# Kernel optimization log

Hardware: AMD Instinct MI355X
Metric: run time of the kernel (lower is better)

Reference implementation:

```python
import jax, jax.numpy as jnp
import numpy as np

N_HEADS = 8
N_LAYERS = 2
LN_EPS = 1e-5


def _mha(x, Win, bin_, Wout, bout):
    # torch nn.MultiheadAttention, eval mode (dropout off). x: [b, s, d]
    b, s, d = x.shape
    dh = d // N_HEADS
    qkv = x @ Win.T + bin_                      # [b, s, 3d]
    q, k, v = jnp.split(qkv, 3, axis=-1)
    q = q.reshape(b, s, N_HEADS, dh)
    k = k.reshape(b, s, N_HEADS, dh)
    v = v.reshape(b, s, N_HEADS, dh)
    scores = jnp.einsum('bqhd,bkhd->bhqk', q, k) / jnp.sqrt(jnp.asarray(dh, x.dtype))
    attn = jax.nn.softmax(scores, axis=-1)
    o = jnp.einsum('bhqk,bkhd->bqhd', attn, v).reshape(b, s, d)
    return o @ Wout.T + bout


def _layer_norm(x, g, b):
    mu = jnp.mean(x, axis=-1, keepdims=True)
    var = jnp.mean(jnp.square(x - mu), axis=-1, keepdims=True)
    return (x - mu) * jax.lax.rsqrt(var + LN_EPS) * g + b


def _vertex_conv(feat, inc, prev, Win, bin_, Wout, bout, Wproj, ln_g, ln_b, alpha):
    # feat: [b,m,d], inc: [b,m,e]
    attn = _mha(feat, Win, bin_, Wout, bout)              # [b,m,d]
    scores = jnp.einsum('bme,bmd->bed', inc, attn)        # incidence aggregation
    w = jax.nn.softmax(scores, axis=1)                    # softmax over edges
    # fused form of einsum('bme,bmd->bmed') then einsum('bmed,bed->bed')
    edge = scores * w                                     # [b,e,d]
    edge = edge @ Wproj.T                                 # no-bias projection
    edge = _layer_norm(edge, ln_g, ln_b)
    if prev is not None:
        edge = alpha * prev + (1.0 - alpha) * edge
        edge = edge + prev
    return edge


def _edge_conv(inc, edge_feat, prev, Win, bin_, Wout, bout, Wproj, ln_g, ln_b, alpha):
    # inc: [b,m,e], edge_feat: [b,e,d]
    _ = _mha(edge_feat, Win, bin_, Wout, bout)            # attn computed, output unused downstream
    wef = jnp.einsum('bed,bme->bmd', edge_feat, inc)      # edge->node aggregation
    node = wef @ Wproj.T
    node = _layer_norm(node, ln_g, ln_b)
    if prev is not None:
        node = alpha * prev + (1.0 - alpha) * node
        node = node + prev
    return node


def setup_inputs() -> dict:
    key = jax.random.key(0)
    ks = jax.random.split(key, 8)
    b, m, e, d = 8, 1024, 1536, 256
    s = 0.02
    return {
        'features': jax.random.normal(ks[0], (b, m, d), jnp.float32),
        'inc_mat': (jax.random.uniform(ks[1], (b, m, e), jnp.float32) < 0.05).astype(jnp.float32),
        'vc_Win': jax.random.normal(ks[2], (3 * d, d), jnp.float32) * s,
        'vc_bin': jnp.zeros((3 * d,), jnp.float32),
        'vc_Wout': jax.random.normal(ks[3], (d, d), jnp.float32) * s,
        'vc_bout': jnp.zeros((d,), jnp.float32),
        'vc_Wproj': jax.random.normal(ks[4], (d, d), jnp.float32) * s,
        'vc_ln_g': jnp.ones((d,), jnp.float32),
        'vc_ln_b': jnp.zeros((d,), jnp.float32),
        'vc_alpha': jnp.asarray(0.5, jnp.float32),
        'ec_Win': jax.random.normal(ks[5], (3 * d, d), jnp.float32) * s,
        'ec_bin': jnp.zeros((3 * d,), jnp.float32),
        'ec_Wout': jax.random.normal(ks[6], (d, d), jnp.float32) * s,
        'ec_bout': jnp.zeros((d,), jnp.float32),
        'ec_Wproj': jax.random.normal(ks[7], (d, d), jnp.float32) * s,
        'ec_ln_g': jnp.ones((d,), jnp.float32),
        'ec_ln_b': jnp.zeros((d,), jnp.float32),
        'ec_alpha': jnp.asarray(0.5, jnp.float32),
    }


def reference(features, inc_mat,
              vc_Win, vc_bin, vc_Wout, vc_bout, vc_Wproj, vc_ln_g, vc_ln_b, vc_alpha,
              ec_Win, ec_bin, ec_Wout, ec_bout, ec_Wproj, ec_ln_g, ec_ln_b, ec_alpha):
    vc = (vc_Win, vc_bin, vc_Wout, vc_bout, vc_Wproj, vc_ln_g, vc_ln_b, vc_alpha)
    ec = (ec_Win, ec_bin, ec_Wout, ec_bout, ec_Wproj, ec_ln_g, ec_ln_b, ec_alpha)
    edge_feats = _vertex_conv(features, inc_mat, None, *vc)
    node_feats = _edge_conv(inc_mat, edge_feats, features, *ec)
    for _ in range(N_LAYERS):  # shared weights across layers, as in the torch module
        edge_feats = _vertex_conv(features, inc_mat, edge_feats, *vc)
        node_feats = _edge_conv(inc_mat, edge_feats, node_feats, *ec)
    return node_feats, edge_feats, inc_mat
```

## Files before the change

### kernel.cpp

```cpp
#include <hip/hip_runtime.h>
#include <stdint.h>


#define DEV static __device__ __forceinline__

typedef __attribute__((ext_vector_type(8))) short bf16x8;
typedef __attribute__((ext_vector_type(4))) float f32x4;

DEV uint16_t f2bf(float x){
  union{float f; uint32_t u;} v; v.f=x;
  uint32_t r = v.u + 0x7fffu + ((v.u>>16)&1u);
  return (uint16_t)(r>>16);
}
DEV float bf2f(uint16_t b){
  union{uint32_t u; float f;} v; v.u=((uint32_t)b)<<16; return v.f;
}

DEV uint32_t cvtpk_bf16(float lo, float hi){
  uint32_t d;
  asm("v_cvt_pk_bf16_f32 %0, %1, %2" : "=v"(d) : "v"(lo), "v"(hi));
  return d;
}

#if __has_builtin(__builtin_amdgcn_exp2f)
DEV float exp2fast(float x){ return __builtin_amdgcn_exp2f(x); }
#else
DEV float exp2fast(float x){ return __expf(x * 0.6931471805599453f); }
#endif

#if __has_builtin(__builtin_amdgcn_global_load_lds)
#define HAVE_GLL 1
#else
#define HAVE_GLL 0
#endif

DEV void load_lds16(const uint16_t* g, void* l){
#if HAVE_GLL
  __builtin_amdgcn_global_load_lds((const __attribute__((address_space(1))) uint32_t*)g,
                                   (__attribute__((address_space(3))) uint32_t*)l, 16, 0, 0);
#else
  *(bf16x8*)l = *(const bf16x8*)g;
#endif
}

__global__ __launch_bounds__(256, 3)
void qkv_prep(const float* __restrict__ inc, float* __restrict__ out_inc,
              uint16_t* __restrict__ incb, uint16_t* __restrict__ incT,
              const float* __restrict__ feats, const float* __restrict__ win,
              const float* __restrict__ bias, uint16_t* __restrict__ qkvb,
              const float* __restrict__ wout, const float* __restrict__ wpv,
              const float* __restrict__ wpe,
              uint16_t* __restrict__ ob_w, uint16_t* __restrict__ ov_w,
              uint16_t* __restrict__ oe_w){
  __shared__ union {
    struct { short As[128*32]; short Bs[128*32]; } g;
    float T[64*65];
  } sm;
  const int tid = threadIdx.x;
  const int bx = blockIdx.x;

  if (bx < 384){
    const int lane = tid & 63;
    const int w = tid >> 6;
    const int wm = w & 1, wn = w >> 1;
    const int r = lane & 15, q = lane >> 4;
    const int mtile = bx & 63, ntile = bx >> 6;
    const float* Fb = feats + (size_t)(mtile*128)*256;
    const float* Wb = win + (size_t)(ntile*128)*256;
    f32x4 acc[4][4];
#pragma unroll
    for (int i=0;i<4;++i)
#pragma unroll
      for (int j=0;j<4;++j) acc[i][j] = (f32x4){0.f,0.f,0.f,0.f};

    const int srow = tid >> 2;
    const int sblk = tid & 3;

    for (int kb = 0; kb < 256; kb += 32){
#pragma unroll
      for (int i=0;i<2;++i){
        int row = srow + 64*i;
        const float* src = Fb + (size_t)row*256 + kb + sblk*8;
        float4 a0 = *(const float4*)src;
        float4 a1 = *(const float4*)(src+4);
        union{uint32_t u[4]; bf16x8 v8;} pk;
        pk.u[0]=cvtpk_bf16(a0.x,a0.y); pk.u[1]=cvtpk_bf16(a0.z,a0.w);
        pk.u[2]=cvtpk_bf16(a1.x,a1.y); pk.u[3]=cvtpk_bf16(a1.z,a1.w);
        *(bf16x8*)&sm.g.As[row*32 + (sblk ^ (row&3))*8] = pk.v8;
      }
#pragma unroll
      for (int i=0;i<2;++i){
        int row = srow + 64*i;
        const float* src = Wb + (size_t)row*256 + kb + sblk*8;
        float4 a0 = *(const float4*)src;
        float4 a1 = *(const float4*)(src+4);
        union{uint32_t u[4]; bf16x8 v8;} pk;
        pk.u[0]=cvtpk_bf16(a0.x,a0.y); pk.u[1]=cvtpk_bf16(a0.z,a0.w);
        pk.u[2]=cvtpk_bf16(a1.x,a1.y); pk.u[3]=cvtpk_bf16(a1.z,a1.w);
        *(bf16x8*)&sm.g.Bs[row*32 + (sblk ^ (row&3))*8] = pk.v8;
      }
      __syncthreads();
      bf16x8 af[4], bfr[4];
#pragma unroll
      for (int mt=0;mt<4;++mt){
        int m = wm*64 + mt*16 + r;
        af[mt] = *(const bf16x8*)&sm.g.As[m*32 + (q ^ (m&3))*8];
      }
#pragma unroll
      for (int nt=0;nt<4;++nt){
        int n = wn*64 + nt*16 + r;
        bfr[nt] = *(const bf16x8*)&sm.g.Bs[n*32 + (q ^ (n&3))*8];
      }
#pragma unroll
      for (int mt=0;mt<4;++mt)
#pragma unroll
        for (int nt=0;nt<4;++nt)
          acc[mt][nt] = __builtin_amdgcn_mfma_f32_16x16x32_bf16(af[mt], bfr[nt], acc[mt][nt], 0,0,0);
      __syncthreads();
    }

    const int gm0 = mtile*128 + wm*64;
    const int gn0 = ntile*128 + wn*64;
#pragma unroll
    for (int mt=0;mt<4;++mt){
#pragma unroll
      for (int nt=0;nt<4;++nt){
        int gn = gn0 + nt*16 + r;
        float bv = bias[gn];
#pragma unroll
        for (int reg=0;reg<4;++reg){
          int gm = gm0 + mt*16 + q*4 + reg;
          qkvb[(size_t)gm*768 + gn] = f2bf(acc[mt][nt][reg] + bv);
        }
      }
    }
  } else if (bx < 3456){
    int p = bx - 384;
    int x = p % 24;
    int t = p / 24;
    int y = t & 15;
    int b = t >> 4;
    int c0 = x*64, r0 = y*64;
    int tx = tid & 15, ty = tid >> 4;
    size_t base = (size_t)b*1024*1536;
#pragma unroll
    for (int jj=0;jj<4;++jj){
      int rl = ty + jj*16;
      size_t idx = base + (size_t)(r0+rl)*1536 + c0 + tx*4;
      float4 v = *(const float4*)&inc[idx];
      *(float4*)&out_inc[idx] = v;
      union{uint16_t u[4]; uint64_t q64;} pk;
      pk.u[0]=f2bf(v.x); pk.u[1]=f2bf(v.y); pk.u[2]=f2bf(v.z); pk.u[3]=f2bf(v.w);
      *(uint64_t*)&incb[idx] = pk.q64;
      float* Tp = &sm.T[rl*65 + tx*4];
      Tp[0]=v.x; Tp[1]=v.y; Tp[2]=v.z; Tp[3]=v.w;
    }
    __syncthreads();
    int c = tid >> 2, ms = (tid & 3) * 16;
    size_t baseT = (size_t)b*1536*1024;
    uint16_t* dst = incT + baseT + (size_t)(c0+c)*1024 + r0 + ms;
    union{uint16_t u[8]; uint4 v4;} o0, o1;
#pragma unroll
    for (int j=0;j<8;++j) o0.u[j] = f2bf(sm.T[(ms+j)*65 + c]);
#pragma unroll
    for (int j=0;j<8;++j) o1.u[j] = f2bf(sm.T[(ms+8+j)*65 + c]);
    *(uint4*)dst = o0.v4;
    *(uint4*)(dst+8) = o1.v4;
  } else {
    int i = (bx - 3456)*256 + tid;
    const float* src; uint16_t* dst; int j;
    if (i < 16384){ src=wout; dst=ob_w; j=i; }
    else if (i < 32768){ src=wpv; dst=ov_w; j=i-16384; }
    else { src=wpe; dst=oe_w; j=i-32768; }
    float4 v = ((const float4*)src)[j];
    union { uint16_t u[4]; uint64_t q; } p;
    p.u[0]=f2bf(v.x); p.u[1]=f2bf(v.y); p.u[2]=f2bf(v.z); p.u[3]=f2bf(v.w);
    ((uint64_t*)dst)[j] = p.q;
  }
}

template<int WM, int BK, int EPI>
__global__ __launch_bounds__(256, 3)
void gemm_nt(const uint16_t* __restrict__ A, const uint16_t* __restrict__ B,
             uint16_t* __restrict__ Cb, const float* __restrict__ bias,
             int M, int N, int K){
  constexpr int AROWS = WM*32;
  constexpr int UPR = BK/8;
  constexpr int RPP = 256/UPR;
  __shared__ short As[AROWS*BK];
  __shared__ short Bs[128*BK];
  const int tid = threadIdx.x;
  const int lane = tid & 63;
  const int w = tid >> 6;
  const int wm = w & 1, wn = w >> 1;
  const int r = lane & 15, q = lane >> 4;
  const uint16_t* Ab = A + (size_t)(blockIdx.x*AROWS)*K;
  const uint16_t* Bb = B + (size_t)(blockIdx.y*128)*K;
  f32x4 acc[WM][4];
#pragma unroll
  for (int i=0;i<WM;++i)
#pragma unroll
    for (int j=0;j<4;++j) acc[i][j] = (f32x4){0.f,0.f,0.f,0.f};

  const int srow = tid / UPR;
  const int sblk = tid % UPR;

  for (int kb = 0; kb < K; kb += BK){
#pragma unroll
    for (int i=0;i<AROWS/RPP;++i){
      int row = srow + RPP*i;
      int lblk = sblk ^ (row & (UPR-1));
      load_lds16(Ab + (size_t)row*K + kb + lblk*8, (char*)As + i*4096 + tid*16);
    }
#pragma unroll
    for (int i=0;i<128/RPP;++i){
      int row = srow + RPP*i;
      int lblk = sblk ^ (row & (UPR-1));
      load_lds16(Bb + (size_t)row*K + kb + lblk*8, (char*)Bs + i*4096 + tid*16);
    }
    __syncthreads();
#pragma unroll
    for (int kc=0;kc<BK/32;++kc){
      bf16x8 af[WM], bfr[4];
#pragma unroll
      for (int mt=0;mt<WM;++mt){
        int m = wm*(WM*16) + mt*16 + r;
        af[mt] = *(const bf16x8*)&As[m*BK + ((kc*4 + q) ^ (m&(UPR-1)))*8];
      }
#pragma unroll
      for (int nt=0;nt<4;++nt){
        int n = wn*64 + nt*16 + r;
        bfr[nt] = *(const bf16x8*)&Bs[n*BK + ((kc*4 + q) ^ (n&(UPR-1)))*8];
      }
#pragma unroll
      for (int mt=0;mt<WM;++mt)
#pragma unroll
        for (int nt=0;nt<4;++nt)
          acc[mt][nt] = __builtin_amdgcn_mfma_f32_16x16x32_bf16(af[mt], bfr[nt], acc[mt][nt], 0,0,0);
    }
    __syncthreads();
  }

  const int gm0 = blockIdx.x*AROWS + wm*(WM*16);
  const int gn0 = blockIdx.y*128 + wn*64;

  if constexpr (EPI == 1){
#pragma unroll
    for (int mt=0;mt<WM;++mt){
      int gmb = gm0 + mt*16 + q*4;
      size_t bb_ = (size_t)(gmb>>10)*(256*1024);
      int mm = gmb & 1023;
#pragma unroll
      for (int nt=0;nt<4;++nt){
        int gn = gn0 + nt*16 + r;
        float bv = bias ? bias[gn] : 0.f;
        union{uint16_t u[4]; uint64_t q64;} pk;
#pragma unroll
        for (int reg=0;reg<4;++reg) pk.u[reg] = f2bf(acc[mt][nt][reg] + bv);
        *(uint64_t*)(Cb + bb_ + (size_t)gn*1024 + mm) = pk.q64;
      }
    }
  } else {
#pragma unroll
    for (int mt=0;mt<WM;++mt){
#pragma unroll
      for (int nt=0;nt<4;++nt){
        int gn = gn0 + nt*16 + r;
        float bv = bias ? bias[gn] : 0.f;
#pragma unroll
        for (int reg=0;reg<4;++reg){
          int gm = gm0 + mt*16 + q*4 + reg;
          Cb[(size_t)gm*N + gn] = f2bf(acc[mt][nt][reg] + bv);
        }
      }
    }
  }
}

__global__ __launch_bounds__(256, 4)
void gemm_score(const uint16_t* __restrict__ A,
                const uint16_t* __restrict__ B,
                float* __restrict__ part,
                uint16_t* __restrict__ VE){
  __shared__ short As[32*64];
  __shared__ short Bs[128*64];
  const int tid = threadIdx.x;
  const int lane = tid & 63;
  const int w = tid >> 6;
  const int r = lane & 15, q = lane >> 4;
  const int bx = (blockIdx.x & 7)*96 + (blockIdx.x >> 3);
  const int batch = bx / 96;
  const int t = bx % 96;
  const int etile = t >> 1, dh = t & 1;
  const uint16_t* Ab = A + (size_t)(batch*1536 + etile*32)*1024;
  const uint16_t* Bb = B + (size_t)(batch*256 + dh*128)*1024;

  f32x4 acc[2][2];
#pragma unroll
  for (int i=0;i<2;++i)
#pragma unroll
    for (int j=0;j<2;++j) acc[i][j] = (f32x4){0.f,0.f,0.f,0.f};

  const int srow = tid >> 3;
  const int sblk = tid & 7;

  for (int kb = 0; kb < 1024; kb += 64){
    { int lblk = sblk ^ (srow & 7);
      load_lds16(Ab + (size_t)srow*1024 + kb + lblk*8, (char*)As + tid*16); }
#pragma unroll
    for (int i=0;i<4;++i){
      int row = srow + 32*i;
      int lblk = sblk ^ (row & 7);
      load_lds16(Bb + (size_t)row*1024 + kb + lblk*8, (char*)Bs + i*4096 + tid*16);
    }
    __syncthreads();
#pragma unroll
    for (int kc=0;kc<2;++kc){
      bf16x8 af[2], bfr[2];
#pragma unroll
      for (int mt=0;mt<2;++mt){
        int m = mt*16 + r;
        af[mt] = *(const bf16x8*)&As[m*64 + ((kc*4 + q) ^ (m&7))*8];
      }
#pragma unroll
      for (int nt=0;nt<2;++nt){
        int n = w*32 + nt*16 + r;
        bfr[nt] = *(const bf16x8*)&Bs[n*64 + ((kc*4 + q) ^ (n&7))*8];
      }
#pragma unroll
      for (int mt=0;mt<2;++mt)
#pragma unroll
        for (int nt=0;nt<2;++nt)
          acc[mt][nt] = __builtin_amdgcn_mfma_f32_16x16x32_bf16(af[mt], bfr[nt], acc[mt][nt], 0,0,0);
    }
    __syncthreads();
  }

  const size_t er0 = (size_t)batch*1536 + etile*32;
#pragma unroll
  for (int nt=0;nt<2;++nt){
    int gn = dh*128 + w*32 + nt*16 + r;
    float s = 0.f;
#pragma unroll
    for (int mt=0;mt<2;++mt){
#pragma unroll
      for (int reg=0;reg<4;++reg){
        float v = acc[mt][nt][reg];
        float ev = __expf(v);
        s += ev;
        int row = mt*16 + q*4 + reg;
        VE[(er0 + row)*256 + gn] = f2bf(v*ev);
      }
    }
    s += __shfl_xor(s, 16);
    s += __shfl_xor(s, 32);
    if (q == 0) part[(size_t)(batch*48 + etile)*256 + gn] = s;
  }
}

__global__ __launch_bounds__(256, 4)
void gemm_ln_edge(const uint16_t* __restrict__ SB, const uint16_t* __restrict__ B,
                  const float* __restrict__ part, const float* __restrict__ g,
                  const float* __restrict__ bb, const float* __restrict__ alpha,
                  float* __restrict__ out, uint16_t* __restrict__ baset){
  __shared__ short As[16*64];
  __shared__ short Bs[256*64];
  __shared__ float lnS[4][16], lnQ[4][16];
  __shared__ float PLinv[256];
  const int tid = threadIdx.x;
  const int lane = tid & 63;
  const int w = tid >> 6;
  const int r = lane & 15, q = lane >> 4;
  const int bx = (blockIdx.x & 7)*96 + (blockIdx.x >> 3);
  const int batch = bx / 96;

  {
    float s = 0.f;
#pragma unroll
    for (int i=0;i<48;++i) s += part[((size_t)batch*48 + i)*256 + tid];
    PLinv[tid] = 1.0f / s;
  }
  __syncthreads();

  f32x4 acc[4];
#pragma unroll
  for (int j=0;j<4;++j) acc[j] = (f32x4){0.f,0.f,0.f,0.f};

  const int srow = tid >> 3;
  const int sblk = tid & 7;

  for (int kb = 0; kb < 256; kb += 64){
    if (tid < 128){
      bf16x8 v = *(const bf16x8*)(SB + (size_t)(bx*16 + srow)*256 + kb + sblk*8);
      const float* Lp = &PLinv[kb + sblk*8];
      float xv[8];
#pragma unroll
      for (int j=0;j<8;++j) xv[j] = bf2f((uint16_t)v[j]) * Lp[j];
      union{uint32_t u[4]; bf16x8 v8;} pk;
      pk.u[0] = cvtpk_bf16(xv[0], xv[1]);
      pk.u[1] = cvtpk_bf16(xv[2], xv[3]);
      pk.u[2] = cvtpk_bf16(xv[4], xv[5]);
      pk.u[3] = cvtpk_bf16(xv[6], xv[7]);
      *(bf16x8*)&As[srow*64 + (sblk ^ (srow&7))*8] = pk.v8;
    }
#pragma unroll
    for (int i=0;i<8;++i){
      int row = srow + 32*i;
      int lblk = sblk ^ (row & 7);
      load_lds16(B + (size_t)row*256 + kb + lblk*8, (char*)Bs + i*4096 + tid*16);
    }
    __syncthreads();
#pragma unroll
    for (int kc=0;kc<2;++kc){
      bf16x8 af, bfr[4];
      { int m = r;
        af = *(const bf16x8*)&As[m*64 + ((kc*4 + q) ^ (m&7))*8]; }
#pragma unroll
      for (int nt=0;nt<4;++nt){
        int n = w*64 + nt*16 + r;
        bfr[nt] = *(const bf16x8*)&Bs[n*64 + ((kc*4 + q) ^ (n&7))*8];
      }
#pragma unroll
      for (int nt=0;nt<4;++nt)
        acc[nt] = __builtin_amdgcn_mfma_f32_16x16x32_bf16(af, bfr[nt], acc[nt], 0,0,0);
    }
    __syncthreads();
  }

  float rs[4], rq[4];
#pragma unroll
  for (int reg=0;reg<4;++reg){
    float s=0.f, s2=0.f;
#pragma unroll
    for (int nt=0;nt<4;++nt){
      float v = acc[nt][reg];
      s += v; s2 += v*v;
    }
#pragma unroll
    for (int off=1; off<16; off<<=1){ s += __shfl_xor(s,off); s2 += __shfl_xor(s2,off); }
    rs[reg]=s; rq[reg]=s2;
  }
  if (r == 0){
#pragma unroll
    for (int reg=0;reg<4;++reg){
      int row = q*4 + reg;
      lnS[w][row] = rs[reg];
      lnQ[w][row] = rq[reg];
    }
  }
  __syncthreads();

  const float c0 = 3.0f + alpha[0];
  float mu_[4], rstd_[4];
#pragma unroll
  for (int reg=0;reg<4;++reg){
    int row = q*4 + reg;
    float S = lnS[0][row]+lnS[1][row]+lnS[2][row]+lnS[3][row];
    float Q = lnQ[0][row]+lnQ[1][row]+lnQ[2][row]+lnQ[3][row];
    float mu = S * (1.f/256.f);
    float var = fmaxf(Q*(1.f/256.f) - mu*mu, 0.f);
    mu_[reg] = mu;
    rstd_[reg] = rsqrtf(var + 1e-5f);
  }

  int e0 = (bx % 96) * 16;
#pragma unroll
  for (int nt=0;nt<4;++nt){
    int gn = w*64 + nt*16 + r;
    float gv = g[gn], bv = bb[gn];
    union{uint16_t u[4]; uint64_t q64;} pk;
#pragma unroll
    for (int reg=0;reg<4;++reg){
      int row = q*4 + reg;
      size_t gm = (size_t)bx*16 + row;
      float o = ((acc[nt][reg]-mu_[reg])*rstd_[reg]*gv + bv) * c0;
      pk.u[reg] = f2bf(o);
      out[gm*256 + gn] = o;
    }
    int ee = e0 + q*4;
    *(uint64_t*)(baset + ((size_t)batch*256 + gn)*1536 + ee) = pk.q64;
  }
}

__global__ __launch_bounds__(256, 3)
void gemm_node_fused(const uint16_t* __restrict__ inc,
                     const uint16_t* __restrict__ baset,
                     const uint16_t* __restrict__ wpe,
                     const float* __restrict__ g, const float* __restrict__ bb,
                     const float* __restrict__ alpha,
                     const float* __restrict__ feats, float* __restrict__ out){
  __shared__ short Ws[256*64];
  __shared__ short As2[16*256];
  __shared__ short Is[16*64];
  const int tid = threadIdx.x;
  const int lane = tid & 63;
  const int w = tid >> 6;
  const int r = lane & 15, q = lane >> 4;
  const int bx = (blockIdx.x & 7)*64 + (blockIdx.x >> 3);
  const int batch = bx >> 6;
  const int mt0 = (bx & 63) * 16;

  const int srow = tid >> 3;
  const int sblk = tid & 7;

  const uint16_t* Bb = baset + (size_t)batch*256*1536;
  const uint16_t* Ib = inc + ((size_t)batch*1024 + mt0)*1536;

  f32x4 acc1[4];
#pragma unroll
  for (int i=0;i<4;++i) acc1[i] = (f32x4){0.f,0.f,0.f,0.f};

  for (int kb = 0; kb < 1536; kb += 64){
#pragma unroll
    for (int i=0;i<8;++i){
      int row = srow + 32*i;
      int lblk = sblk ^ (row & 7);
      load_lds16(Bb + (size_t)row*1536 + kb + lblk*8, (char*)Ws + i*4096 + tid*16);
    }
    if (tid < 128){
      int lblk = sblk ^ (srow & 7);
      load_lds16(Ib + (size_t)srow*1536 + kb + lblk*8, (char*)Is + tid*16);
    }
    __syncthreads();
#pragma unroll
    for (int kc=0;kc<2;++kc){
      bf16x8 af[4], bfr;
#pragma unroll
      for (int mt=0;mt<4;++mt){
        int d = w*64 + mt*16 + r;
        af[mt] = *(const bf16x8*)&Ws[d*64 + ((kc*4 + q) ^ (d&7))*8];
      }
      { int m = r;
        bfr = *(const bf16x8*)&Is[m*64 + ((kc*4 + q) ^ (m&7))*8]; }
#pragma unroll
      for (int mt=0;mt<4;++mt)
        acc1[mt] = __builtin_amdgcn_mfma_f32_16x16x32_bf16(af[mt], bfr, acc1[mt], 0,0,0);
    }
    __syncthreads();
  }

#pragma unroll
  for (int mt=0;mt<4;++mt){
    int j = w*8 + mt*2 + (q>>1);
    int m = r;
    union{uint16_t u[4]; uint64_t q64;} pk;
#pragma unroll
    for (int reg=0;reg<4;++reg) pk.u[reg] = f2bf(acc1[mt][reg]);
    *(uint64_t*)((char*)As2 + m*512 + ((j ^ (m&7))<<4) + ((q&1)<<3)) = pk.q64;
  }

  f32x4 acc2[4];
#pragma unroll
  for (int i=0;i<4;++i) acc2[i] = (f32x4){0.f,0.f,0.f,0.f};

  for (int kb = 0; kb < 256; kb += 64){
#pragma unroll
    for (int i=0;i<8;++i){
      int row = srow + 32*i;
      int lblk = sblk ^ (row & 7);
      load_lds16(wpe + (size_t)row*256 + kb + lblk*8, (char*)Ws + i*4096 + tid*16);
    }
    __syncthreads();
#pragma unroll
    for (int kc=0;kc<2;++kc){
      bf16x8 af[4], bfr;
#pragma unroll
      for (int mt=0;mt<4;++mt){
        int dp = w*64 + mt*16 + r;
        af[mt] = *(const bf16x8*)&Ws[dp*64 + ((kc*4 + q) ^ (dp&7))*8];
      }
      { int m = r;
        int jr = (kb>>3) + kc*4 + q;
        bfr = *(const bf16x8*)((char*)As2 + m*512 + ((jr ^ (m&7))<<4)); }
#pragma unroll
      for (int mt=0;mt<4;++mt)
        acc2[mt] = __builtin_amdgcn_mfma_f32_16x16x32_bf16(af[mt], bfr, acc2[mt], 0,0,0);
    }
    __syncthreads();
  }

  float* lnS = (float*)Is;
  float* lnQ = lnS + 64;
  float s_, q_;
  {
    float s=0.f, s2=0.f;
#pragma unroll
    for (int mt=0;mt<4;++mt)
#pragma unroll
      for (int reg=0;reg<4;++reg){
        float v = acc2[mt][reg];
        s += v; s2 += v*v;
      }
    s += __shfl_xor(s,16); s2 += __shfl_xor(s2,16);
    s += __shfl_xor(s,32); s2 += __shfl_xor(s2,32);
    s_ = s; q_ = s2;
  }
  if (q == 0){
    lnS[w*16 + r] = s_;
    lnQ[w*16 + r] = q_;
  }
  __syncthreads();

  const float a = alpha[0];
  const float ap1 = 1.f + a;
  const float cn = (1.f - a)*(ap1*ap1 + ap1 + 1.f);
  const float cf = ap1*ap1*ap1;

  float mu_, rstd_;
  {
    int col = r;
    float S = lnS[col] + lnS[16+col] + lnS[32+col] + lnS[48+col];
    float Q = lnQ[col] + lnQ[16+col] + lnQ[32+col] + lnQ[48+col];
    float mu = S * (1.f/256.f);
    float var = fmaxf(Q*(1.f/256.f) - mu*mu, 0.f);
    mu_ = mu;
    rstd_ = rsqrtf(var + 1e-5f);
  }

#pragma unroll
  for (int mt=0;mt<4;++mt){
    int dp0 = w*64 + mt*16 + q*4;
    float4 gv = *(const float4*)&g[dp0];
    float4 bv = *(const float4*)&bb[dp0];
    int m = r;
    size_t gm = (size_t)batch*1024 + mt0 + m;
    float4 fv = *(const float4*)&feats[gm*256 + dp0];
    float4 ov;
    ov.x = cf*fv.x + cn*((acc2[mt][0]-mu_)*rstd_*gv.x + bv.x);
    ov.y = cf*fv.y + cn*((acc2[mt][1]-mu_)*rstd_*gv.y + bv.y);
    ov.z = cf*fv.z + cn*((acc2[mt][2]-mu_)*rstd_*gv.z + bv.z);
    ov.w = cf*fv.w + cn*((acc2[mt][3]-mu_)*rstd_*gv.w + bv.w);
    *(float4*)&out[gm*256 + dp0] = ov;
  }
}

DEV void stage_K(short* Kl, const uint16_t* __restrict__ qkv, size_t rowbase,
                 int c, int h, int kr){
  const uint16_t* kp = qkv + ((rowbase + c*256 + kr)*768 + 256 + h*32);
  int sz = (kr&3) ^ ((kr>>2)&1);
#pragma unroll
  for (int lb=0; lb<4; ++lb){
    bf16x8 v = *(const bf16x8*)(kp + lb*8);
    *(bf16x8*)&Kl[kr*32 + ((lb ^ sz))*8] = v;
  }
}

DEV void stage_V(short* VT, const uint16_t* __restrict__ qkv, size_t rowbase,
                 int c, int h, int t){
  int kvp = (t>>1)*2;
  int dhh = (t&1)*16;
  const uint16_t* v0 = qkv + ((rowbase + c*256 + kvp)*768 + 512 + h*32 + dhh);
  const uint16_t* v1 = v0 + 768;
  bf16x8 a0 = *(const bf16x8*)(v0);
  bf16x8 a1 = *(const bf16x8*)(v0+8);
  bf16x8 b0 = *(const bf16x8*)(v1);
  bf16x8 b1 = *(const bf16x8*)(v1+8);
  int blkbase = kvp>>3, off = kvp&7;
#pragma unroll
  for (int i=0;i<8;++i){
    int dh = dhh + i;
    uint32_t pack = (uint32_t)(uint16_t)a0[i] | ((uint32_t)(uint16_t)b0[i]<<16);
    *(uint32_t*)&VT[dh*256 + ((blkbase ^ (dh&7))*8) + off] = pack;
  }
#pragma unroll
  for (int i=0;i<8;++i){
    int dh = dhh + 8 + i;
    uint32_t pack = (uint32_t)(uint16_t)a1[i] | ((uint32_t)(uint16_t)b1[i]<<16);
    *(uint32_t*)&VT[dh*256 + ((blkbase ^ (dh&7))*8) + off] = pack;
  }
}

__global__ __launch_bounds__(512)
void attn_fwd(const uint16_t* __restrict__ qkv, uint16_t* __restrict__ O){
  __shared__ short Kl[256*32];
  __shared__ short VT[32*256];
  __shared__ short Pl[8][16*36];
  const int tid = threadIdx.x, lane = tid&63, w = tid>>6;
  const int r = lane&15, q = lane>>4;
  const int logical = (blockIdx.x & 7)*64 + (blockIdx.x >> 3);
  const int bh = logical >> 3, qc = logical & 7;
  const int b = bh>>3, h = bh&7;
  const int q0 = qc*128 + w*16;
  const size_t rowbase = (size_t)b*1024;

  bf16x8 aq;
  {
    const float qscale = 0.25505654380651023f;
    const uint16_t* p = qkv + ((rowbase + q0 + r)*768 + h*32 + q*8);
    bf16x8 t = *(const bf16x8*)p;
#pragma unroll
    for (int j=0;j<8;++j)
      t[j] = (short)f2bf(bf2f((uint16_t)t[j]) * qscale);
    aq = t;
  }

  f32x4 o[2];
  o[0]=(f32x4){0.f,0.f,0.f,0.f}; o[1]=(f32x4){0.f,0.f,0.f,0.f};
  float l = 0.f;

  for (int c=0;c<4;++c){
    __syncthreads();
    if (tid < 256) stage_K(Kl, qkv, rowbase, c, h, tid);
    else           stage_V(VT, qkv, rowbase, c, h, tid-256);
    __syncthreads();
    for (int s32=0; s32<8; ++s32){
#pragma unroll
      for (int t2=0;t2<2;++t2){
        int rn = s32*32 + t2*16 + r;
        int sz = (rn&3) ^ ((rn>>2)&1);
        bf16x8 bk = *(const bf16x8*)&Kl[rn*32 + ((q ^ sz))*8];
        f32x4 z = (f32x4){0.f,0.f,0.f,0.f};
        __builtin_amdgcn_s_setprio(1);
        f32x4 st = __builtin_amdgcn_mfma_f32_16x16x32_bf16(bk, aq, z, 0,0,0);
        __builtin_amdgcn_s_setprio(0);
        float p0 = exp2fast(st[0]);
        float p1 = exp2fast(st[1]);
        float p2 = exp2fast(st[2]);
        float p3 = exp2fast(st[3]);
        l += (p0+p1)+(p2+p3);
        union{uint32_t u[2]; uint64_t q64;} pk;
        pk.u[0] = cvtpk_bf16(p0, p1);
        pk.u[1] = cvtpk_bf16(p2, p3);
        *(uint64_t*)&Pl[w][r*36 + t2*16 + q*4] = pk.q64;
      }
      bf16x8 bv[2];
#pragma unroll
      for (int db=0;db<2;++db){
        int dh = db*16 + r;
        bv[db] = *(const bf16x8*)&VT[dh*256 + (((s32*4 + q) ^ (dh&7)))*8];
      }
      bf16x8 ap = *(const bf16x8*)&Pl[w][r*36 + q*8];
      __builtin_amdgcn_s_setprio(1);
#pragma unroll
      for (int db=0;db<2;++db)
        o[db] = __builtin_amdgcn_mfma_f32_16x16x32_bf16(ap, bv[db], o[db], 0,0,0);
      __builtin_amdgcn_s_setprio(0);
    }
  }

  l += __shfl_xor(l, 16);
  l += __shfl_xor(l, 32);
#pragma unroll
  for (int db=0;db<2;++db)
#pragma unroll
    for (int reg=0;reg<4;++reg){
      float li = __shfl(l, q*4 + reg);
      int qr = q0 + q*4 + reg;
      O[(rowbase + qr)*256 + h*32 + db*16 + r] = f2bf(o[db][reg] / li);
    }
}

extern "C" void kernel_launch(void* const* d_in, const int* in_sizes, int n_in,
                              void* d_out, int out_size, void* d_ws, size_t ws_size,
                              hipStream_t stream){
  const float* features = (const float*)d_in[0];
  const float* inc      = (const float*)d_in[1];
  const float* vc_Win   = (const float*)d_in[2];
  const float* vc_bin   = (const float*)d_in[3];
  const float* vc_Wout  = (const float*)d_in[4];
  const float* vc_bout  = (const float*)d_in[5];
  const float* vc_Wproj = (const float*)d_in[6];
  const float* vc_ln_g  = (const float*)d_in[7];
  const float* vc_ln_b  = (const float*)d_in[8];
  const float* vc_alpha = (const float*)d_in[9];
  const float* ec_Wproj = (const float*)d_in[14];
  const float* ec_ln_g  = (const float*)d_in[15];
  const float* ec_ln_b  = (const float*)d_in[16];
  const float* ec_alpha = (const float*)d_in[17];

  float* out = (float*)d_out;
  float* out_node = out;
  float* out_edge = out + 2097152;
  float* out_inc  = out + 5242880;

  char* ws = (char*)d_ws;
  float*    PART   = (float*)   (ws + 0);
  uint16_t* WOUTB  = (uint16_t*)(ws + 4587520);
  uint16_t* WPVB   = (uint16_t*)(ws + 4718592);
  uint16_t* WPEB   = (uint16_t*)(ws + 4849664);
  uint16_t* INCB   = (uint16_t*)(ws + 4988928);
  uint16_t* INCT   = (uint16_t*)(ws + 30154752);
  uint16_t* QKVB   = (uint16_t*)(ws + 55320576);
  uint16_t* SCORESB= (uint16_t*)(ws + 55320576);
  uint16_t* OB     = (uint16_t*)(ws + 67903488);
  uint16_t* ATTNT  = (uint16_t*)(ws + 72097792);
  uint16_t* BASET  = (uint16_t*)(ws + 82583552);

  qkv_prep<<<3648,256,0,stream>>>(inc, out_inc, INCB, INCT,
                                  features, vc_Win, vc_bin, QKVB,
                                  vc_Wout, vc_Wproj, ec_Wproj,
                                  WOUTB, WPVB, WPEB);

  attn_fwd<<<512,512,0,stream>>>(QKVB, OB);
  gemm_nt<2,128,1><<<dim3(128,2,1),256,0,stream>>>(OB, WOUTB, ATTNT, vc_bout,
                                                   8192,256,256);

  gemm_score<<<768,256,0,stream>>>(INCT, ATTNT, PART, SCORESB);

  gemm_ln_edge<<<768,256,0,stream>>>(SCORESB, WPVB, PART, vc_ln_g, vc_ln_b,
                                     vc_alpha, out_edge, BASET);

  gemm_node_fused<<<512,256,0,stream>>>(INCB, BASET, WPEB, ec_ln_g, ec_ln_b,
                                        ec_alpha, features, out_node);
}
```

Measured before the change: 242.1 us.

## Reassociate out-projection after incidence aggregation and fuse into score GEMM

Drops the separate out-projection GEMM. The incidence aggregation now multiplies the attention output O directly, (inc^T O) Wout^T, and the bias term is recovered as column sums of inc times bout. Those column sums are computed in the prep kernel, and attn_fwd writes O transposed through LDS. The score kernel chains two MFMA GEMMs per 16-edge tile, so the per-block B tile doubles to 256 columns. This removes one launch and the ATTNT round trip, in exchange for extra K=256 GEMM work per edge tile and a larger LDS footprint.

New measurement: 251.4 us. 3.8% more time.

```diff
diff --git a/kernel.cpp b/kernel.cpp
--- a/kernel.cpp
+++ b/kernel.cpp
@@ -51,7 +51,8 @@
               const float* __restrict__ wout, const float* __restrict__ wpv,
               const float* __restrict__ wpe,
               uint16_t* __restrict__ ob_w, uint16_t* __restrict__ ov_w,
-              uint16_t* __restrict__ oe_w){
+              uint16_t* __restrict__ oe_w,
+              float* __restrict__ incpart){
   __shared__ union {
     struct { short As[128*32]; short Bs[128*32]; } g;
     float T[64*65];
@@ -160,12 +161,17 @@
     size_t baseT = (size_t)b*1536*1024;
     uint16_t* dst = incT + baseT + (size_t)(c0+c)*1024 + r0 + ms;
     union{uint16_t u[8]; uint4 v4;} o0, o1;
-#pragma unroll
-    for (int j=0;j<8;++j) o0.u[j] = f2bf(sm.T[(ms+j)*65 + c]);
-#pragma unroll
-    for (int j=0;j<8;++j) o1.u[j] = f2bf(sm.T[(ms+8+j)*65 + c]);
+    float csum = 0.f;
+#pragma unroll
+    for (int j=0;j<8;++j){ float v = sm.T[(ms+j)*65 + c]; csum += v; o0.u[j] = f2bf(v); }
+#pragma unroll
+    for (int j=0;j<8;++j){ float v = sm.T[(ms+8+j)*65 + c]; csum += v; o1.u[j] = f2bf(v); }
     *(uint4*)dst = o0.v4;
     *(uint4*)(dst+8) = o1.v4;
+    csum += __shfl_xor(csum, 1);
+    csum += __shfl_xor(csum, 2);
+    if ((tid & 3) == 0)
+      incpart[((size_t)(b*16 + y))*1536 + c0 + c] = csum;
   } else {
     int i = (bx - 3456)*256 + tid;
     const float* src; uint16_t* dst; int j;
@@ -179,136 +185,51 @@
   }
 }
 
-template<int WM, int BK, int EPI>
 __global__ __launch_bounds__(256, 3)
-void gemm_nt(const uint16_t* __restrict__ A, const uint16_t* __restrict__ B,
-             uint16_t* __restrict__ Cb, const float* __restrict__ bias,
-             int M, int N, int K){
-  constexpr int AROWS = WM*32;
-  constexpr int UPR = BK/8;
-  constexpr int RPP = 256/UPR;
-  __shared__ short As[AROWS*BK];
-  __shared__ short Bs[128*BK];
-  const int tid = threadIdx.x;
-  const int lane = tid & 63;
-  const int w = tid >> 6;
-  const int wm = w & 1, wn = w >> 1;
-  const int r = lane & 15, q = lane >> 4;
-  const uint16_t* Ab = A + (size_t)(blockIdx.x*AROWS)*K;
-  const uint16_t* Bb = B + (size_t)(blockIdx.y*128)*K;
-  f32x4 acc[WM][4];
-#pragma unroll
-  for (int i=0;i<WM;++i)
-#pragma unroll
-    for (int j=0;j<4;++j) acc[i][j] = (f32x4){0.f,0.f,0.f,0.f};
-
-  const int srow = tid / UPR;
-  const int sblk = tid % UPR;
-
-  for (int kb = 0; kb < K; kb += BK){
-#pragma unroll
-    for (int i=0;i<AROWS/RPP;++i){
-      int row = srow + RPP*i;
-      int lblk = sblk ^ (row & (UPR-1));
-      load_lds16(Ab + (size_t)row*K + kb + lblk*8, (char*)As + i*4096 + tid*16);
-    }
-#pragma unroll
-    for (int i=0;i<128/RPP;++i){
-      int row = srow + RPP*i;
-      int lblk = sblk ^ (row & (UPR-1));
-      load_lds16(Bb + (size_t)row*K + kb + lblk*8, (char*)Bs + i*4096 + tid*16);
-    }
-    __syncthreads();
-#pragma unroll
-    for (int kc=0;kc<BK/32;++kc){
-      bf16x8 af[WM], bfr[4];
-#pragma unroll
-      for (int mt=0;mt<WM;++mt){
-        int m = wm*(WM*16) + mt*16 + r;
-        af[mt] = *(const bf16x8*)&As[m*BK + ((kc*4 + q) ^ (m&(UPR-1)))*8];
-      }
-#pragma unroll
-      for (int nt=0;nt<4;++nt){
-        int n = wn*64 + nt*16 + r;
-        bfr[nt] = *(const bf16x8*)&Bs[n*BK + ((kc*4 + q) ^ (n&(UPR-1)))*8];
-      }
-#pragma unroll
-      for (int mt=0;mt<WM;++mt)
-#pragma unroll
-        for (int nt=0;nt<4;++nt)
-          acc[mt][nt] = __builtin_amdgcn_mfma_f32_16x16x32_bf16(af[mt], bfr[nt], acc[mt][nt], 0,0,0);
-    }
-    __syncthreads();
-  }
-
-  const int gm0 = blockIdx.x*AROWS + wm*(WM*16);
-  const int gn0 = blockIdx.y*128 + wn*64;
-
-  if constexpr (EPI == 1){
-#pragma unroll
-    for (int mt=0;mt<WM;++mt){
-      int gmb = gm0 + mt*16 + q*4;
-      size_t bb_ = (size_t)(gmb>>10)*(256*1024);
-      int mm = gmb & 1023;
-#pragma unroll
-      for (int nt=0;nt<4;++nt){
-        int gn = gn0 + nt*16 + r;
-        float bv = bias ? bias[gn] : 0.f;
-        union{uint16_t u[4]; uint64_t q64;} pk;
-#pragma unroll
-        for (int reg=0;reg<4;++reg) pk.u[reg] = f2bf(acc[mt][nt][reg] + bv);
-        *(uint64_t*)(Cb + bb_ + (size_t)gn*1024 + mm) = pk.q64;
-      }
-    }
-  } else {
-#pragma unroll
-    for (int mt=0;mt<WM;++mt){
-#pragma unroll
-      for (int nt=0;nt<4;++nt){
-        int gn = gn0 + nt*16 + r;
-        float bv = bias ? bias[gn] : 0.f;
-#pragma unroll
-        for (int reg=0;reg<4;++reg){
-          int gm = gm0 + mt*16 + q*4 + reg;
-          Cb[(size_t)gm*N + gn] = f2bf(acc[mt][nt][reg] + bv);
-        }
-      }
-    }
-  }
-}
-
-__global__ __launch_bounds__(256, 4)
-void gemm_score(const uint16_t* __restrict__ A,
-                const uint16_t* __restrict__ B,
-                float* __restrict__ part,
-                uint16_t* __restrict__ VE){
-  __shared__ short As[32*64];
-  __shared__ short Bs[128*64];
+void gemm_score_fused(const uint16_t* __restrict__ A,
+                      const uint16_t* __restrict__ OT,
+                      const uint16_t* __restrict__ woutb,
+                      const float* __restrict__ bout,
+                      const float* __restrict__ incpart,
+                      float* __restrict__ part,
+                      uint16_t* __restrict__ VE){
+  __shared__ short As[16*64];
+  __shared__ short Bs[256*64];
+  __shared__ short As2[16*256];
+  __shared__ float incsum[16];
   const int tid = threadIdx.x;
   const int lane = tid & 63;
   const int w = tid >> 6;
   const int r = lane & 15, q = lane >> 4;
   const int bx = (blockIdx.x & 7)*96 + (blockIdx.x >> 3);
   const int batch = bx / 96;
-  const int t = bx % 96;
-  const int etile = t >> 1, dh = t & 1;
-  const uint16_t* Ab = A + (size_t)(batch*1536 + etile*32)*1024;
-  const uint16_t* Bb = B + (size_t)(batch*256 + dh*128)*1024;
-
-  f32x4 acc[2][2];
-#pragma unroll
-  for (int i=0;i<2;++i)
-#pragma unroll
-    for (int j=0;j<2;++j) acc[i][j] = (f32x4){0.f,0.f,0.f,0.f};
+  const int etile = bx % 96;
+
+  if (tid < 16){
+    float s = 0.f;
+#pragma unroll
+    for (int y=0;y<16;++y)
+      s += incpart[((size_t)(batch*16 + y))*1536 + etile*16 + tid];
+    incsum[tid] = s;
+  }
+
+  const uint16_t* Ab = A + (size_t)(batch*1536 + etile*16)*1024;
+  const uint16_t* Bb = OT + (size_t)batch*256*1024;
+
+  f32x4 acc1[4];
+#pragma unroll
+  for (int i=0;i<4;++i) acc1[i] = (f32x4){0.f,0.f,0.f,0.f};
 
   const int srow = tid >> 3;
   const int sblk = tid & 7;
 
   for (int kb = 0; kb < 1024; kb += 64){
-    { int lblk = sblk ^ (srow & 7);
-      load_lds16(Ab + (size_t)srow*1024 + kb + lblk*8, (char*)As + tid*16); }
-#pragma unroll
-    for (int i=0;i<4;++i){
+    if (tid < 128){
+      int lblk = sblk ^ (srow & 7);
+      load_lds16(Ab + (size_t)srow*1024 + kb + lblk*8, (char*)As + tid*16);
+    }
+#pragma unroll
+    for (int i=0;i<8;++i){
       int row = srow + 32*i;
       int lblk = sblk ^ (row & 7);
       load_lds16(Bb + (size_t)row*1024 + kb + lblk*8, (char*)Bs + i*4096 + tid*16);
@@ -316,45 +237,89 @@
     __syncthreads();
 #pragma unroll
     for (int kc=0;kc<2;++kc){
-      bf16x8 af[2], bfr[2];
-#pragma unroll
-      for (int mt=0;mt<2;++mt){
-        int m = mt*16 + r;
-        af[mt] = *(const bf16x8*)&As[m*64 + ((kc*4 + q) ^ (m&7))*8];
-      }
-#pragma unroll
-      for (int nt=0;nt<2;++nt){
-        int n = w*32 + nt*16 + r;
-        bfr[nt] = *(const bf16x8*)&Bs[n*64 + ((kc*4 + q) ^ (n&7))*8];
-      }
-#pragma unroll
-      for (int mt=0;mt<2;++mt)
-#pragma unroll
-        for (int nt=0;nt<2;++nt)
-          acc[mt][nt] = __builtin_amdgcn_mfma_f32_16x16x32_bf16(af[mt], bfr[nt], acc[mt][nt], 0,0,0);
-    }
-    __syncthreads();
-  }
-
-  const size_t er0 = (size_t)batch*1536 + etile*32;
-#pragma unroll
-  for (int nt=0;nt<2;++nt){
-    int gn = dh*128 + w*32 + nt*16 + r;
-    float s = 0.f;
-#pragma unroll
-    for (int mt=0;mt<2;++mt){
-#pragma unroll
-      for (int reg=0;reg<4;++reg){
-        float v = acc[mt][nt][reg];
-        float ev = __expf(v);
-        s += ev;
-        int row = mt*16 + q*4 + reg;
-        VE[(er0 + row)*256 + gn] = f2bf(v*ev);
-      }
-    }
-    s += __shfl_xor(s, 16);
-    s += __shfl_xor(s, 32);
-    if (q == 0) part[(size_t)(batch*48 + etile)*256 + gn] = s;
+      bf16x8 af[4], bfr;
+#pragma unroll
+      for (int mt=0;mt<4;++mt){
+        int j = w*64 + mt*16 + r;
+        af[mt] = *(const bf16x8*)&Bs[j*64 + ((kc*4 + q) ^ (j&7))*8];
+      }
+      { int e = r;
+        bfr = *(const bf16x8*)&As[e*64 + ((kc*4 + q) ^ (e&7))*8]; }
+#pragma unroll
+      for (int mt=0;mt<4;++mt)
+        acc1[mt] = __builtin_amdgcn_mfma_f32_16x16x32_bf16(af[mt], bfr, acc1[mt], 0,0,0);
+    }
+    __syncthreads();
+  }
+
+#pragma unroll
+  for (int mt=0;mt<4;++mt){
+    int J = w*8 + mt*2 + (q>>1);
+    int e = r;
+    union{uint16_t u[4]; uint64_t q64;} pk;
+#pragma unroll
+    for (int reg=0;reg<4;++reg) pk.u[reg] = f2bf(acc1[mt][reg]);
+    *(uint64_t*)((char*)As2 + e*512 + ((J ^ (e&7))<<4) + ((q&1)<<3)) = pk.q64;
+  }
+
+  f32x4 acc2[4];
+#pragma unroll
+  for (int i=0;i<4;++i) acc2[i] = (f32x4){0.f,0.f,0.f,0.f};
+
+  for (int kb = 0; kb < 256; kb += 64){
+#pragma unroll
+    for (int i=0;i<8;++i){
+      int row = srow + 32*i;
+      int lblk = sblk ^ (row & 7);
+      load_lds16(woutb + (size_t)row*256 + kb + lblk*8, (char*)Bs + i*4096 + tid*16);
+    }
+    __syncthreads();
+#pragma unroll
+    for (int kc=0;kc<2;++kc){
+      bf16x8 af[4], bfr;
+#pragma unroll
+      for (int mt=0;mt<4;++mt){
+        int d = w*64 + mt*16 + r;
+        af[mt] = *(const bf16x8*)&Bs[d*64 + ((kc*4 + q) ^ (d&7))*8];
+      }
+      { int e = r;
+        int Jr = (kb>>3) + kc*4 + q;
+        bfr = *(const bf16x8*)((char*)As2 + e*512 + ((Jr ^ (e&7))<<4)); }
+#pragma unroll
+      for (int mt=0;mt<4;++mt)
+        acc2[mt] = __builtin_amdgcn_mfma_f32_16x16x32_bf16(af[mt], bfr, acc2[mt], 0,0,0);
+    }
+    __syncthreads();
+  }
+
+  const size_t er = (size_t)batch*1536 + etile*16 + r;
+  const float isum = incsum[r];
+#pragma unroll
+  for (int mt=0;mt<4;++mt){
+    int d0 = w*64 + mt*16 + q*4;
+    float4 bo = *(const float4*)&bout[d0];
+    float sv[4], ev[4];
+#pragma unroll
+    for (int reg=0;reg<4;++reg){
+      float bvv = (reg==0)?bo.x:(reg==1)?bo.y:(reg==2)?bo.z:bo.w;
+      float v = acc2[mt][reg] + isum*bvv;
+      float e = __expf(v);
+      sv[reg] = v*e; ev[reg] = e;
+    }
+    union{uint16_t u[4]; uint64_t q64;} pk;
+#pragma unroll
+    for (int reg=0;reg<4;++reg) pk.u[reg] = f2bf(sv[reg]);
+    *(uint64_t*)(VE + er*256 + d0) = pk.q64;
+#pragma unroll
+    for (int reg=0;reg<4;++reg){
+      float s = ev[reg];
+      s += __shfl_xor(s, 1);
+      s += __shfl_xor(s, 2);
+      s += __shfl_xor(s, 4);
+      s += __shfl_xor(s, 8);
+      if (r == 0)
+        part[((size_t)(batch*96 + etile))*256 + d0 + reg] = s;
+    }
   }
 }
 
@@ -377,7 +342,7 @@
   {
     float s = 0.f;
 #pragma unroll
-    for (int i=0;i<48;++i) s += part[((size_t)batch*48 + i)*256 + tid];
+    for (int i=0;i<96;++i) s += part[((size_t)batch*96 + i)*256 + tid];
     PLinv[tid] = 1.0f / s;
   }
   __syncthreads();
@@ -671,7 +636,7 @@
 }
 
 __global__ __launch_bounds__(512)
-void attn_fwd(const uint16_t* __restrict__ qkv, uint16_t* __restrict__ O){
+void attn_fwd(const uint16_t* __restrict__ qkv, uint16_t* __restrict__ OT){
   __shared__ short Kl[256*32];
   __shared__ short VT[32*256];
   __shared__ short Pl[8][16*36];
@@ -740,14 +705,27 @@
 
   l += __shfl_xor(l, 16);
   l += __shfl_xor(l, 32);
-#pragma unroll
-  for (int db=0;db<2;++db)
+
+  short* Ob = &Pl[0][0];
+  __syncthreads();
+#pragma unroll
+  for (int db=0; db<2; ++db){
+    union{uint16_t u[4]; uint64_t q64;} pk;
 #pragma unroll
     for (int reg=0;reg<4;++reg){
       float li = __shfl(l, q*4 + reg);
-      int qr = q0 + q*4 + reg;
-      O[(rowbase + qr)*256 + h*32 + db*16 + r] = f2bf(o[db][reg] / li);
-    }
+      pk.u[reg] = f2bf(o[db][reg] / li);
+    }
+    int j = db*16 + r;
+    int u = w*4 + q;
+    *(uint64_t*)((char*)Ob + j*256 + ((u ^ ((j&7)<<2))<<3)) = pk.q64;
+  }
+  __syncthreads();
+  {
+    int row = tid >> 4, i = tid & 15;
+    uint4 v = *(const uint4*)((char*)Ob + row*256 + (((2*i) ^ ((row&7)<<2))<<3));
+    *(uint4*)&OT[((size_t)(b*256 + h*32 + row))*1024 + qc*128 + i*8] = v;
+  }
 }
 
 extern "C" void kernel_launch(void* const* d_in, const int* in_sizes, int n_in,
@@ -775,6 +753,7 @@
 
   char* ws = (char*)d_ws;
   float*    PART   = (float*)   (ws + 0);
+  float*    INCPART= (float*)   (ws + 1048576);
   uint16_t* WOUTB  = (uint16_t*)(ws + 4587520);
   uint16_t* WPVB   = (uint16_t*)(ws + 4718592);
   uint16_t* WPEB   = (uint16_t*)(ws + 4849664);
@@ -782,20 +761,18 @@
   uint16_t* INCT   = (uint16_t*)(ws + 30154752);
   uint16_t* QKVB   = (uint16_t*)(ws + 55320576);
   uint16_t* SCORESB= (uint16_t*)(ws + 55320576);
-  uint16_t* OB     = (uint16_t*)(ws + 67903488);
-  uint16_t* ATTNT  = (uint16_t*)(ws + 72097792);
+  uint16_t* OT     = (uint16_t*)(ws + 67903488);
   uint16_t* BASET  = (uint16_t*)(ws + 82583552);
 
   qkv_prep<<<3648,256,0,stream>>>(inc, out_inc, INCB, INCT,
                                   features, vc_Win, vc_bin, QKVB,
                                   vc_Wout, vc_Wproj, ec_Wproj,
-                                  WOUTB, WPVB, WPEB);
-
-  attn_fwd<<<512,512,0,stream>>>(QKVB, OB);
-  gemm_nt<2,128,1><<<dim3(128,2,1),256,0,stream>>>(OB, WOUTB, ATTNT, vc_bout,
-                                                   8192,256,256);
-
-  gemm_score<<<768,256,0,stream>>>(INCT, ATTNT, PART, SCORESB);
+                                  WOUTB, WPVB, WPEB, INCPART);
+
+  attn_fwd<<<512,512,0,stream>>>(QKVB, OT);
+
+  gemm_score_fused<<<768,256,0,stream>>>(INCT, OT, WOUTB, vc_bout,
+                                         INCPART, PART, SCORESB);
 
   gemm_ln_edge<<<768,256,0,stream>>>(SCORESB, WPVB, PART, vc_ln_g, vc_ln_b,
                                      vc_alpha, out_edge, BASET);
```
